# Kernel optimization log

Measured on AMD Instinct MI355X. Metric: run time of the kernel, lower is better.

The kernel has to match this reference:

```python
import jax, jax.numpy as jnp
import numpy as np

B, T, D = 2, 2048, 2048
H, DH = 32, 64
GN_EPS = DH * 1e-5  # GroupNorm eps = head_dim * norm_eps


def _lora(x, A, Bm, bias, act):
    h = x @ A.T
    if act == 'tanh':
        h = jnp.tanh(h)
    elif act == 'sigmoid':
        h = jax.nn.sigmoid(h)
    y = h @ Bm.T
    if bias is not None:
        y = y + bias
    return y


def setup_inputs() -> dict:
    key = jax.random.key(0)
    ks = jax.random.split(key, 24)
    def nrm(i, shape, s):
        return jax.random.normal(ks[i], shape, jnp.float32) * s
    return {
        'hidden_states': nrm(0, (B, T, D), 1.0),
        'v_state': nrm(1, (B, T, D), 1.0),
        'x_x': nrm(2, (6, D), 0.3),
        'k_k': 0.85 + nrm(3, (D,), 0.05),
        'k_a': 1.0 + nrm(4, (D,), 0.05),
        'r_k': nrm(5, (H, DH), 0.1),
        'Wr': nrm(6, (D, D), 0.02),
        'Wk': nrm(7, (D, D), 0.02),
        'Wv': nrm(8, (D, D), 0.02),
        'Wo': nrm(9, (D, D), 0.02),
        'wA': nrm(10, (64, D), 0.02), 'wB': nrm(11, (D, 64), 0.02), 'wb': nrm(12, (D,), 0.5),
        'vA': nrm(13, (16, D), 0.02), 'vB': nrm(14, (D, 16), 0.02), 'vb': jnp.zeros((D,), jnp.float32),
        'aA': nrm(15, (64, D), 0.02), 'aB': nrm(16, (D, 64), 0.02), 'ab': jnp.zeros((D,), jnp.float32),
        'gA': nrm(17, (128, D), 0.02), 'gB': nrm(18, (D, 128), 0.02),
        'gn_w': jnp.ones((D,), jnp.float32), 'gn_b': jnp.zeros((D,), jnp.float32),
    }


def reference(hidden_states, v_state, x_x, k_k, k_a, r_k, Wr, Wk, Wv, Wo,
              wA, wB, wb, vA, vB, vb, aA, aB, ab, gA, gB, gn_w, gn_b):
    b, t, d = hidden_states.shape
    # time_shift: shifted[t] = x[t-1], shifted[0] = 0
    shifted = jnp.pad(hidden_states, ((0, 0), (1, 0), (0, 0)))[:, :t]
    delta = shifted - hidden_states
    xm = hidden_states[None] + delta[None] * x_x[:, None, None, :]  # [6,B,T,D]
    xr, xw, xk, xv, xa, xg = xm[0], xm[1], xm[2], xm[3], xm[4], xm[5]

    r = xr @ Wr.T
    w = -jax.nn.softplus(-_lora(xw, wA, wB, wb, 'tanh')) - 0.5  # log decay, < -0.5
    k = xk @ Wk.T
    v = xv @ Wv.T
    # layer_idx != 0: v = lerp(v, v_state, sigmoid(v_lora(xv)))
    v = v + jax.nn.sigmoid(_lora(xv, vA, vB, vb, None)) * (v_state - v)
    a = jax.nn.sigmoid(_lora(xa, aA, aB, ab, None))
    g = _lora(xg, gA, gB, None, 'sigmoid')

    kk = (k * k_k).reshape(b, t, H, DH)
    kk = kk / jnp.maximum(jnp.linalg.norm(kk, axis=-1, keepdims=True), 1e-12)
    k = k * (1.0 + (a - 1.0) * k_a)

    r_h = r.reshape(b, t, H, DH)
    w_h = w.reshape(b, t, H, DH)
    k_h = k.reshape(b, t, H, DH)
    v_h = v.reshape(b, t, H, DH)
    a_h = a.reshape(b, t, H, DH)
    tm = lambda x: jnp.swapaxes(x, 0, 1)  # [B,T,H,DH] -> [T,B,H,DH]

    # RWKV7 DPLR delta rule: S = diag(exp(w)) S; S += b (a^T S) + k v^T; o = r^T S
    def step(S, xs):
        q_t, w_t, k_t, v_t, at, bt = xs  # each [B,H,DH]
        S = S * jnp.exp(w_t)[..., None]
        sa = jnp.einsum('bhk,bhkv->bhv', at, S)
        S = S + bt[..., None] * sa[..., None, :] + k_t[..., None] * v_t[..., None, :]
        return S, jnp.einsum('bhk,bhkv->bhv', q_t, S)

    S0 = jnp.zeros((b, H, DH, DH), hidden_states.dtype)
    _, o = jax.lax.scan(step, S0,
                        (tm(r_h), tm(w_h), tm(k_h), tm(v_h), tm(-kk), tm(kk * a_h)))
    o = jnp.swapaxes(o, 0, 1)  # [B,T,H,DH]

    # GroupNorm over each head's channels
    mu = o.mean(-1, keepdims=True)
    var = jnp.mean((o - mu) ** 2, axis=-1, keepdims=True)
    on = ((o - mu) / jnp.sqrt(var + GN_EPS)).reshape(b, t, d) * gn_w + gn_b

    on = on + ((r_h * k_h * r_k).sum(-1, keepdims=True) * v_h).reshape(b, t, d)
    return (on * g) @ Wo.T
```

## Files before the change

### kernel.cpp

```cpp
#include <hip/hip_runtime.h>
#include <hip/hip_bf16.h>
#include <math.h>


typedef __attribute__((ext_vector_type(8))) unsigned short ushort8;
typedef __attribute__((ext_vector_type(8))) _Float16 f16x8;
typedef __attribute__((ext_vector_type(4))) float f32x4;
typedef __attribute__((ext_vector_type(2))) float f32x2;

__device__ inline unsigned short f2h(float f) {
    _Float16 h = (_Float16)f;
    return __builtin_bit_cast(unsigned short, h);
}
__device__ inline float h2f(unsigned short u) {
    return (float)__builtin_bit_cast(_Float16, u);
}
__device__ inline float sigm(float x) { return 1.f / (1.f + expf(-x)); }

template <int CTRL>
__device__ __forceinline__ float rrot(float x) {
    int xi = __builtin_bit_cast(int, x);
    int yi = __builtin_amdgcn_update_dpp(xi, xi, CTRL, 0xf, 0xf, true);
    return x + __builtin_bit_cast(float, yi);
}
__device__ __forceinline__ float red8(float x)  { return rrot<0x128>(x); }
__device__ __forceinline__ float red16(float x) {
    float b = x;
    asm("" : "+v"(b));
    float a = x;
    asm("v_permlane16_swap_b32 %0, %1" : "+v"(a), "+v"(b));
    return a + b;
}
__device__ __forceinline__ float red32(float x) {
    float b = x;
    asm("" : "+v"(b));
    float a = x;
    asm("v_permlane32_swap_b32 %0, %1" : "+v"(a), "+v"(b));
    return a + b;
}
__device__ __forceinline__ float full64(float x) {
    x = rrot<0x121>(x);
    x = rrot<0x122>(x);
    x = rrot<0x124>(x);
    x = rrot<0x128>(x);
    return red32(red16(x));
}

__device__ __forceinline__ void gld16(void* lds, const void* g)
{
    __builtin_amdgcn_global_load_lds(
        (const __attribute__((address_space(1))) void*)g,
        (__attribute__((address_space(3))) void*)lds, 16, 0, 0);
}
__device__ __forceinline__ void gld4(void* lds, const void* g)
{
    __builtin_amdgcn_global_load_lds(
        (const __attribute__((address_space(1))) void*)g,
        (__attribute__((address_space(3))) void*)lds, 4, 0, 0);
}

__global__ void mixcvt_h(const float* __restrict__ in, const float* __restrict__ xxr,
                         unsigned short* __restrict__ o16, int T, int D, int total8, int domix)
{
    int i = blockIdx.x * 256 + threadIdx.x;
    if (i >= total8) return;
    const size_t e = (size_t)i * 8;
    float a[8];
    *(float4*)&a[0] = *(const float4*)(in + e);
    *(float4*)&a[4] = *(const float4*)(in + e + 4);
    if (domix) {
        const int m = (int)(e / D);
        const int d = (int)(e % D);
        const int t = m % T;
        float p[8] = {0.f,0.f,0.f,0.f,0.f,0.f,0.f,0.f};
        if (t > 0) {
            *(float4*)&p[0] = *(const float4*)(in + e - D);
            *(float4*)&p[4] = *(const float4*)(in + e - D + 4);
        }
        float xv[8];
        *(float4*)&xv[0] = *(const float4*)(xxr + d);
        *(float4*)&xv[4] = *(const float4*)(xxr + d + 4);
        #pragma unroll
        for (int j = 0; j < 8; ++j) a[j] += (p[j] - a[j]) * xv[j];
    }
    ushort8 o;
    #pragma unroll
    for (int j = 0; j < 8; ++j) o[j] = f2h(a[j]);
    *(ushort8*)(o16 + e) = o;
}

__global__ void mixcvt2_h(const float* __restrict__ in,
                          const float* __restrict__ xx0, const float* __restrict__ xx1,
                          unsigned short* __restrict__ o0, unsigned short* __restrict__ o1,
                          int T, int D, int total8)
{
    int i = blockIdx.x * 256 + threadIdx.x;
    if (i >= total8) return;
    const size_t e = (size_t)i * 8;
    float a[8];
    *(float4*)&a[0] = *(const float4*)(in + e);
    *(float4*)&a[4] = *(const float4*)(in + e + 4);
    const int m = (int)(e / D);
    const int d = (int)(e % D);
    const int t = m % T;
    float p[8] = {0.f,0.f,0.f,0.f,0.f,0.f,0.f,0.f};
    if (t > 0) {
        *(float4*)&p[0] = *(const float4*)(in + e - D);
        *(float4*)&p[4] = *(const float4*)(in + e - D + 4);
    }
    float x0[8], x1[8];
    *(float4*)&x0[0] = *(const float4*)(xx0 + d);
    *(float4*)&x0[4] = *(const float4*)(xx0 + d + 4);
    *(float4*)&x1[0] = *(const float4*)(xx1 + d);
    *(float4*)&x1[4] = *(const float4*)(xx1 + d + 4);
    ushort8 r0, r1;
    #pragma unroll
    for (int j = 0; j < 8; ++j) {
        r0[j] = f2h(a[j] + (p[j] - a[j]) * x0[j]);
        r1[j] = f2h(a[j] + (p[j] - a[j]) * x1[j]);
    }
    *(ushort8*)(o0 + e) = r0;
    *(ushort8*)(o1 + e) = r1;
}

__global__ void wsplit_h(const float* __restrict__ in,
                         unsigned short* __restrict__ hi, unsigned short* __restrict__ lo,
                         int total8)
{
    int i = blockIdx.x * 256 + threadIdx.x;
    if (i >= total8) return;
    const size_t e = (size_t)i * 8;
    float a[8];
    *(float4*)&a[0] = *(const float4*)(in + e);
    *(float4*)&a[4] = *(const float4*)(in + e + 4);
    ushort8 h8, l8;
    #pragma unroll
    for (int j = 0; j < 8; ++j) {
        const unsigned short h = f2h(a[j]);
        h8[j] = h;
        l8[j] = f2h(a[j] - h2f(h));
    }
    *(ushort8*)(hi + e) = h8;
    *(ushort8*)(lo + e) = l8;
}

__global__ void wcvt_h(const float* __restrict__ in,
                       unsigned short* __restrict__ hi, int total8)
{
    int i = blockIdx.x * 256 + threadIdx.x;
    if (i >= total8) return;
    const size_t e = (size_t)i * 8;
    float a[8];
    *(float4*)&a[0] = *(const float4*)(in + e);
    *(float4*)&a[4] = *(const float4*)(in + e + 4);
    ushort8 h8;
    #pragma unroll
    for (int j = 0; j < 8; ++j) h8[j] = f2h(a[j]);
    *(ushort8*)(hi + e) = h8;
}

#define GBM 128
#define GBN 128

template <int TERMS>
__global__ __launch_bounds__(256) void gemm_h2(
    const unsigned short* __restrict__ Ag,
    const unsigned short* __restrict__ Bhg, const unsigned short* __restrict__ Blg,
    float* __restrict__ C, int M, int N, int K, int mode,
    const float* __restrict__ yv, const float* __restrict__ bias,
    const float* __restrict__ aux,
    size_t sA, size_t sB, size_t sC)
{
    __shared__ unsigned short As[GBM * 32];
    __shared__ unsigned short Bhs[GBN * 32], Bls[GBN * 32];
    const int z = blockIdx.z;
    Ag  += (size_t)z * sA;
    Bhg += (size_t)z * sB;
    Blg += (size_t)z * sB;
    C   += (size_t)z * sC;
    const int tid = threadIdx.x;
    const int m0 = blockIdx.x * GBM;
    const int n0 = blockIdx.y * GBN;
    const int wave = tid >> 6, lane = tid & 63;
    const int wr = (wave >> 1) * 64, wc = (wave & 1) * 64;
    const int fr = lane & 15, fq = lane >> 4;

    f32x4 acc[4][4];
    #pragma unroll
    for (int i = 0; i < 4; ++i)
        #pragma unroll
        for (int j = 0; j < 4; ++j)
            acc[i][j] = (f32x4){0.f, 0.f, 0.f, 0.f};

    const unsigned short* gsrc;
    unsigned short* lbuf;
    int rofs, nld;
    if (wave == 0)      { gsrc = Ag;  lbuf = As;           rofs = m0;      nld = 4; }
    else if (wave == 1) { gsrc = Ag;  lbuf = As + 64 * 32; rofs = m0 + 64; nld = 4; }
    else if (wave == 2) { gsrc = Bhg; lbuf = Bhs;          rofs = n0;      nld = 8; }
    else                { gsrc = Blg; lbuf = Bls;          rofs = n0;      nld = (TERMS == 2) ? 8 : 0; }
    const unsigned short* gbase = gsrc + (size_t)(rofs + (lane >> 2)) * K + ((lane & 3) << 3);

    for (int k0 = 0; k0 < K; k0 += 32) {
        #pragma unroll
        for (int j = 0; j < 8; ++j)
            if (j < nld)
                gld16(lbuf + j * 16 * 32, gbase + (size_t)(j * 16) * K + k0);
        __syncthreads();

        f16x8 fa[4], fbh[4], fbl[4];
        #pragma unroll
        for (int m = 0; m < 4; ++m)
            fa[m] = *(const f16x8*)&As[(wr + m * 16 + fr) * 32 + fq * 8];
        #pragma unroll
        for (int n = 0; n < 4; ++n) {
            fbh[n] = *(const f16x8*)&Bhs[(wc + n * 16 + fr) * 32 + fq * 8];
            if constexpr (TERMS == 2)
                fbl[n] = *(const f16x8*)&Bls[(wc + n * 16 + fr) * 32 + fq * 8];
        }
        #pragma unroll
        for (int m = 0; m < 4; ++m)
            #pragma unroll
            for (int n = 0; n < 4; ++n) {
                acc[m][n] = __builtin_amdgcn_mfma_f32_16x16x32_f16(fa[m], fbh[n], acc[m][n], 0, 0, 0);
                if constexpr (TERMS == 2)
                    acc[m][n] = __builtin_amdgcn_mfma_f32_16x16x32_f16(fa[m], fbl[n], acc[m][n], 0, 0, 0);
            }
        __syncthreads();
    }

    #pragma unroll
    for (int m = 0; m < 4; ++m) {
        const int row = m0 + wr + m * 16 + fq * 4;
        #pragma unroll
        for (int n = 0; n < 4; ++n) {
            const int col = n0 + wc + n * 16 + fr;
            #pragma unroll
            for (int j = 0; j < 4; ++j) {
                const size_t idx = (size_t)(row + j) * N + col;
                float v = acc[m][n][j];
                if (mode == 2) {
                    const float sg = sigm(yv[idx] + bias[col]);
                    v = v + sg * (aux[idx] - v);
                }
                C[idx] = v;
            }
        }
    }
}

#define BM 64
#define BN 64
#define BK 16
__global__ __launch_bounds__(256) void gemm_f32(
    const float* __restrict__ A, const float* __restrict__ xx,
    const float* __restrict__ W, float* __restrict__ C,
    int M, int N, int K, int T, int mode, const float* __restrict__ bias)
{
    __shared__ float As[BK][BM + 4];
    __shared__ float Bs[BK][BN + 4];
    const int tid = threadIdx.x;
    const int m0 = blockIdx.x * BM;
    const int n0 = blockIdx.y * BN;
    const int lr = tid >> 2;
    const int lk = (tid & 3) << 2;
    const int tx = tid & 15;
    const int ty = tid >> 4;
    const int mrow = m0 + lr;
    const int nrow = n0 + lr;
    float acc[4][4];
    #pragma unroll
    for (int i = 0; i < 4; ++i)
        #pragma unroll
        for (int j = 0; j < 4; ++j) acc[i][j] = 0.f;

    for (int k0 = 0; k0 < K; k0 += BK) {
        const float* ap = A + (size_t)mrow * K + k0 + lk;
        float4 av = *(const float4*)ap;
        if (xx) {
            const int t = mrow % T;
            float4 pv = make_float4(0.f, 0.f, 0.f, 0.f);
            if (t > 0) pv = *(const float4*)(ap - K);
            const float4 xv = *(const float4*)(xx + k0 + lk);
            av.x += (pv.x - av.x) * xv.x;
            av.y += (pv.y - av.y) * xv.y;
            av.z += (pv.z - av.z) * xv.z;
            av.w += (pv.w - av.w) * xv.w;
        }
        float4 bv = make_float4(0.f, 0.f, 0.f, 0.f);
        if (nrow < N) bv = *(const float4*)(W + (size_t)nrow * K + k0 + lk);

        As[lk + 0][lr] = av.x; As[lk + 1][lr] = av.y;
        As[lk + 2][lr] = av.z; As[lk + 3][lr] = av.w;
        Bs[lk + 0][lr] = bv.x; Bs[lk + 1][lr] = bv.y;
        Bs[lk + 2][lr] = bv.z; Bs[lk + 3][lr] = bv.w;
        __syncthreads();

        #pragma unroll
        for (int kk = 0; kk < BK; ++kk) {
            const float4 a4 = *(const float4*)&As[kk][ty << 2];
            const float4 b4 = *(const float4*)&Bs[kk][tx << 2];
            const float a[4] = {a4.x, a4.y, a4.z, a4.w};
            const float b[4] = {b4.x, b4.y, b4.z, b4.w};
            #pragma unroll
            for (int i = 0; i < 4; ++i)
                #pragma unroll
                for (int j = 0; j < 4; ++j)
                    acc[i][j] = fmaf(a[i], b[j], acc[i][j]);
        }
        __syncthreads();
    }
    #pragma unroll
    for (int i = 0; i < 4; ++i) {
        const int m = m0 + (ty << 2) + i;
        #pragma unroll
        for (int j = 0; j < 4; ++j) {
            const int n = n0 + (tx << 2) + j;
            if (n < N) {
                const size_t idx = (size_t)m * N + n;
                float v = acc[i][j];
                if (mode == 1) v = 0.6065306597126334f * sigm(v + bias[n]);
                C[idx] = v;
            }
        }
    }
}

__global__ __launch_bounds__(256) void lora1(
    const float* __restrict__ hid, const float* __restrict__ x_x,
    const float* __restrict__ wA, const float* __restrict__ vA,
    const float* __restrict__ aA, const float* __restrict__ gA,
    float* __restrict__ HW, float* __restrict__ HV,
    float* __restrict__ HA, float* __restrict__ HG,
    int M, int K, int T)
{
    __shared__ float As[BK][BM + 4];
    __shared__ float Bs[BK][BN + 4];
    const int y = blockIdx.y;
    const float* W; const float* xx; float* C; int NL, act, nofs, nvalid;
    if (y == 0)      { W = wA; xx = x_x + 1 * (size_t)K; C = HW; NL = 64;  act = 1; nofs = 0;  nvalid = 64; }
    else if (y == 1) { W = vA; xx = x_x + 3 * (size_t)K; C = HV; NL = 16;  act = 0; nofs = 0;  nvalid = 16; }
    else if (y == 2) { W = aA; xx = x_x + 4 * (size_t)K; C = HA; NL = 64;  act = 0; nofs = 0;  nvalid = 64; }
    else             { W = gA + (size_t)(y - 3) * 64 * K; xx = x_x + 5 * (size_t)K; C = HG; NL = 128; act = 2; nofs = (y - 3) * 64; nvalid = 64; }

    const int tid = threadIdx.x;
    const int m0 = blockIdx.x * BM;
    const int lr = tid >> 2;
    const int lk = (tid & 3) << 2;
    const int tx = tid & 15;
    const int ty = tid >> 4;
    const int mrow = m0 + lr;
    float acc[4][4];
    #pragma unroll
    for (int i = 0; i < 4; ++i)
        #pragma unroll
        for (int j = 0; j < 4; ++j) acc[i][j] = 0.f;

    for (int k0 = 0; k0 < K; k0 += BK) {
        const float* ap = hid + (size_t)mrow * K + k0 + lk;
        float4 av = *(const float4*)ap;
        {
            const int t = mrow % T;
            float4 pv = make_float4(0.f, 0.f, 0.f, 0.f);
            if (t > 0) pv = *(const float4*)(ap - K);
            const float4 xv = *(const float4*)(xx + k0 + lk);
            av.x += (pv.x - av.x) * xv.x;
            av.y += (pv.y - av.y) * xv.y;
            av.z += (pv.z - av.z) * xv.z;
            av.w += (pv.w - av.w) * xv.w;
        }
        float4 bv = make_float4(0.f, 0.f, 0.f, 0.f);
        if (lr < nvalid) bv = *(const float4*)(W + (size_t)lr * K + k0 + lk);

        As[lk + 0][lr] = av.x; As[lk + 1][lr] = av.y;
        As[lk + 2][lr] = av.z; As[lk + 3][lr] = av.w;
        Bs[lk + 0][lr] = bv.x; Bs[lk + 1][lr] = bv.y;
        Bs[lk + 2][lr] = bv.z; Bs[lk + 3][lr] = bv.w;
        __syncthreads();

        #pragma unroll
        for (int kk = 0; kk < BK; ++kk) {
            const float4 a4 = *(const float4*)&As[kk][ty << 2];
            const float4 b4 = *(const float4*)&Bs[kk][tx << 2];
            const float a[4] = {a4.x, a4.y, a4.z, a4.w};
            const float b[4] = {b4.x, b4.y, b4.z, b4.w};
            #pragma unroll
            for (int i = 0; i < 4; ++i)
                #pragma unroll
                for (int j = 0; j < 4; ++j)
                    acc[i][j] = fmaf(a[i], b[j], acc[i][j]);
        }
        __syncthreads();
    }
    #pragma unroll
    for (int i = 0; i < 4; ++i) {
        const int m = m0 + (ty << 2) + i;
        #pragma unroll
        for (int j = 0; j < 4; ++j) {
            const int n = (tx << 2) + j;
            if (n < nvalid) {
                float v = acc[i][j];
                if (act == 1) v = tanhf(v);
                else if (act == 2) v = sigm(v);
                C[(size_t)m * NL + nofs + n] = v;
            }
        }
    }
}

__global__ __launch_bounds__(256) void ka_epi(
    float* __restrict__ Kf, float* __restrict__ A_BV, float* __restrict__ KKo,
    const float* __restrict__ k_k, const float* __restrict__ k_a,
    const float* __restrict__ ab, int total, int H)
{
    int wid = (blockIdx.x << 2) | (threadIdx.x >> 6);
    if (wid >= total) return;
    const int l = threadIdx.x & 63;
    const int h = wid % H;
    const int ch = h * 64 + l;
    const size_t base = (size_t)wid * 64;
    float k0 = Kf[base + l];
    float a = sigm(A_BV[base + l] + ab[ch]);
    float kkr = k0 * k_k[ch];
    float ss = full64(kkr * kkr);
    float inv = 1.f / fmaxf(sqrtf(ss), 1e-12f);
    float kkn = kkr * inv;
    KKo[base + l] = kkn;
    A_BV[base + l] = kkn * a;
    Kf[base + l] = k0 * fmaf(a - 1.f, k_a[ch], 1.f);
}

#define SCH 16
__global__ __launch_bounds__(64) void rwkv_scan(
    const float* __restrict__ EW, const float* __restrict__ R,
    const float* __restrict__ Kf, const float* __restrict__ Vf,
    const float* __restrict__ KK, const float* __restrict__ BV,
    float* __restrict__ O, int T, int H)
{
    __shared__ float lds[2][5 * SCH * 64 + SCH * 8];

    const int blk = blockIdx.x;
    const int bh = blk & 63;
    const int slab = blk >> 6;
    const int b = bh >> 5, h = bh & 31;
    const int l = threadIdx.x;
    const int vc = l & 7;
    const int g  = l >> 3;
    const int kb = g << 3;
    const int vb0 = slab << 3;
    const size_t step = (size_t)H * 64;
    const size_t base0 = ((size_t)b * T * H + h) * 64;

    auto stage = [&](int c, int buf) {
        float* L = &lds[buf][0];
        const size_t t0 = (size_t)c * SCH;
        const float* gs[5] = {EW, R, Kf, KK, BV};
        #pragma unroll
// ... 47 lines not shown
                const f32x2 qlo = __builtin_shufflevector(pp.q[j], pp.q[j], 0, 1);
                const f32x2 qhi = __builtin_shufflevector(pp.q[j], pp.q[j], 2, 3);
                s2[2*j]   *= elo;
                s2[2*j+1] *= ehi;
                sa0 += qlo * s2[2*j];
                sa1 += qhi * s2[2*j+1];
            }
            const f32x2 sas = sa0 + sa1;
            float p = -(sas.x + sas.y);
            p = red32(red16(red8(p)));
            const f32x2 p2 = (f32x2){p, p};
            const f32x2 v2 = (f32x2){pp.vv, pp.vv};
            f32x2 o0 = (f32x2){0.f, 0.f}, o1 = (f32x2){0.f, 0.f};
            #pragma unroll
            for (int j = 0; j < 2; ++j) {
                const f32x2 klo = __builtin_shufflevector(pp.k[j], pp.k[j], 0, 1);
                const f32x2 khi = __builtin_shufflevector(pp.k[j], pp.k[j], 2, 3);
                const f32x2 blo = __builtin_shufflevector(pp.bb[j], pp.bb[j], 0, 1);
                const f32x2 bhi = __builtin_shufflevector(pp.bb[j], pp.bb[j], 2, 3);
                const f32x2 rlo = __builtin_shufflevector(pp.r[j], pp.r[j], 0, 1);
                const f32x2 rhi = __builtin_shufflevector(pp.r[j], pp.r[j], 2, 3);
                s2[2*j]   = blo * p2 + (klo * v2 + s2[2*j]);
                s2[2*j+1] = bhi * p2 + (khi * v2 + s2[2*j+1]);
                o0 += rlo * s2[2*j];
                o1 += rhi * s2[2*j+1];
            }
            const f32x2 os = o0 + o1;
            float oo = os.x + os.y;
            oo = red32(red16(red8(oo)));
            if (g == 0)
                O[base0 + (size_t)(c * SCH + tt) * step + vb0 + vc] = oo;
        };

        PRE(PA, 0);
        PRE(PB, 1);
        #pragma unroll
        for (int tt = 0; tt < SCH - 2; tt += 2) {
            COMP(PA, tt);     PRE(PA, tt + 2);
            COMP(PB, tt + 1); PRE(PB, tt + 3);
        }
        COMP(PA, SCH - 2);
        COMP(PB, SCH - 1);

        asm volatile("s_waitcnt vmcnt(0)" ::: "memory");
        __builtin_amdgcn_sched_barrier(0);
    }
}

__global__ __launch_bounds__(256) void gn_bonus(
    const float* __restrict__ O, const float* __restrict__ R,
    const float* __restrict__ Kf, const float* __restrict__ Vf,
    const float* __restrict__ G, const float* __restrict__ r_k,
    const float* __restrict__ gn_w, const float* __restrict__ gn_b,
    float* __restrict__ ON, int total, int H, float eps)
{
    int wid = (blockIdx.x << 2) | (threadIdx.x >> 6);
    if (wid >= total) return;
    const int l = threadIdx.x & 63;
    const int h = wid % H;
    const int ch = h * 64 + l;
    const size_t base = (size_t)wid * 64;

    const float o = O[base + l];
    const float mu = full64(o) * (1.f / 64.f);
    const float d = o - mu;
    const float ss = full64(d * d);
    const float inv = 1.f / sqrtf(ss * (1.f / 64.f) + eps);
    float on = d * inv * gn_w[ch] + gn_b[ch];

    const float r = R[base + l], k = Kf[base + l], vv = Vf[base + l];
    const float p = full64(r * k * r_k[ch]);
    on = fmaf(p, vv, on);
    ON[base + l] = on * G[base + l];
}

extern "C" void kernel_launch(void* const* d_in, const int* in_sizes, int n_in,
                              void* d_out, int out_size, void* d_ws, size_t ws_size,
                              hipStream_t stream)
{
    const int B = 2, T = 2048, D = 2048, H = 32;
    const int M = B * T;

    const float* hid = (const float*)d_in[0];
    const float* vst = (const float*)d_in[1];
    const float* x_x = (const float*)d_in[2];
    const float* k_k = (const float*)d_in[3];
    const float* k_a = (const float*)d_in[4];
    const float* r_k = (const float*)d_in[5];
    const float* Wr  = (const float*)d_in[6];
    const float* Wk  = (const float*)d_in[7];
    const float* Wv  = (const float*)d_in[8];
    const float* Wo  = (const float*)d_in[9];
    const float* wA  = (const float*)d_in[10];
    const float* wB  = (const float*)d_in[11];
    const float* wb  = (const float*)d_in[12];
    const float* vA  = (const float*)d_in[13];
    const float* vB  = (const float*)d_in[14];
    const float* vb  = (const float*)d_in[15];
    const float* aA  = (const float*)d_in[16];
    const float* aB  = (const float*)d_in[17];
    const float* ab  = (const float*)d_in[18];
    const float* gA  = (const float*)d_in[19];
    const float* gB  = (const float*)d_in[20];
    const float* gnw = (const float*)d_in[21];
    const float* gnb = (const float*)d_in[22];
    float* out = (float*)d_out;

    const size_t NE = (size_t)M * D;
    const size_t DD = (size_t)D * D;
    const size_t need = (6 * NE + (size_t)M * 272) * sizeof(float);
    if (ws_size < need) return;

    float* R_  = (float*)d_ws;
    float* EW  = R_  + NE;
    float* Kf  = EW  + NE;
    float* Vf  = Kf  + NE;
    float* KK  = Vf  + NE;
    float* ABV = KK  + NE;
    float* HW  = ABV + NE;
    float* HV  = HW + (size_t)M * 64;
    float* HA  = HV + (size_t)M * 16;
    float* HG  = HA + (size_t)M * 64;

    dim3 blk(256);
    const int nMix = (int)(NE / 8);
    const int nW   = (int)(DD / 8);
    const float* nf = nullptr;

    hipLaunchKernelGGL(lora1, dim3(M / BM, 5), blk, 0, stream,
                       hid, x_x, wA, vA, aA, gA, HW, HV, HA, HG, M, D, T);

    hipLaunchKernelGGL(gemm_f32, dim3(M / BM, D / BN), blk, 0, stream, HV, nf, vB, ABV, M, D, 16, T, 0, nf);

    unsigned short* X2  = (unsigned short*)EW;
    unsigned short* W2  = (unsigned short*)KK;
    hipLaunchKernelGGL(mixcvt2_h, dim3(nMix / 256), blk, 0, stream,
                       hid, x_x + 0 * (size_t)D, x_x + 2 * (size_t)D, X2, X2 + NE, T, D, nMix);
    hipLaunchKernelGGL(wcvt_h, dim3(nW / 256), blk, 0, stream, Wr, W2, nW);
    hipLaunchKernelGGL(wcvt_h, dim3(nW / 256), blk, 0, stream, Wk, W2 + DD, nW);
    hipLaunchKernelGGL((gemm_h2<1>), dim3(M / GBM, D / GBN, 2), blk, 0, stream,
                       X2, W2, W2, R_, M, D, D, 0, nf, nf, nf,
                       NE, DD, 2 * NE);

    hipLaunchKernelGGL(mixcvt_h, dim3(nMix / 256), blk, 0, stream, hid, x_x + 3 * (size_t)D, X2, T, D, nMix, 1);
    hipLaunchKernelGGL(wcvt_h, dim3(nW / 256), blk, 0, stream, Wv, W2, nW);
    hipLaunchKernelGGL((gemm_h2<1>), dim3(M / GBM, D / GBN, 1), blk, 0, stream,
                       X2, W2, W2, Vf, M, D, D, 2, ABV, vb, vst, 0, 0, 0);

    hipLaunchKernelGGL(gemm_f32, dim3(M / BM, D / BN), blk, 0, stream, HW, nf, wB, EW,  M, D, 64, T, 1, wb);
    hipLaunchKernelGGL(gemm_f32, dim3(M / BM, D / BN), blk, 0, stream, HA, nf, aB, ABV, M, D, 64, T, 0, nf);

    const int totalW = M * H;
    hipLaunchKernelGGL(ka_epi, dim3(totalW / 4), blk, 0, stream, Kf, ABV, KK, k_k, k_a, ab, totalW, H);

    hipLaunchKernelGGL(rwkv_scan, dim3(B * H * 8), dim3(64), 0, stream, EW, R_, Kf, Vf, KK, ABV, out, T, H);

    unsigned short* HG16 = (unsigned short*)ABV;
    unsigned short* gbHi = HG16 + (size_t)M * 128;
    unsigned short* gbLo = gbHi + (size_t)D * 128;
    float* G_ = KK;
    hipLaunchKernelGGL(mixcvt_h, dim3((M * 128 / 8) / 256), blk, 0, stream, HG, nf, HG16, T, D, M * 128 / 8, 0);
    hipLaunchKernelGGL(wsplit_h, dim3((D * 128 / 8) / 256), blk, 0, stream, gB, gbHi, gbLo, D * 128 / 8);
    hipLaunchKernelGGL((gemm_h2<2>), dim3(M / GBM, D / GBN, 1), blk, 0, stream,
                       HG16, gbHi, gbLo, G_, M, D, 128, 0, nf, nf, nf, 0, 0, 0);
    hipLaunchKernelGGL(gn_bonus, dim3(totalW / 4), blk, 0, stream, out, R_, Kf, Vf, G_, r_k, gnw, gnb, EW, totalW, H, 64.f * 1e-5f);

    unsigned short* ON16 = (unsigned short*)KK;
    unsigned short* WoHi = (unsigned short*)ABV;
    unsigned short* WoLo = WoHi + DD;
    hipLaunchKernelGGL(mixcvt_h, dim3(nMix / 256), blk, 0, stream, EW, nf, ON16, T, D, nMix, 0);
    hipLaunchKernelGGL(wsplit_h, dim3(nW / 256), blk, 0, stream, Wo, WoHi, WoLo, nW);
    hipLaunchKernelGGL((gemm_h2<2>), dim3(M / GBM, D / GBN, 1), blk, 0, stream,
                       ON16, WoHi, WoLo, out, M, D, D, 0, nf, nf, nf, 0, 0, 0);
}
```

Measured before the change: 1.005 ms.

## Fuse fp16 conversions into producer epilogues and batch small kernels

The gate-LoRA hidden state is now written as fp16 straight from lora1, and gn_bonus writes its output as fp16. This removes two separate mixcvt conversion passes and the fp32 round trip through memory that each one needed. The two weight conversions for Wr/Wk are merged into one launch, and the w/a LoRA second-stage GEMMs run in one launch using a z-grid. Buffer aliasing is reshuffled so ON16 lives in EW and HG16 sits in the small workspace region.

```diff
diff --git a/kernel.cpp b/kernel.cpp
--- a/kernel.cpp
+++ b/kernel.cpp
@@ -144,11 +144,14 @@
     *(ushort8*)(lo + e) = l8;
 }
 
-__global__ void wcvt_h(const float* __restrict__ in,
-                       unsigned short* __restrict__ hi, int total8)
+__global__ void wcvt2_h(const float* __restrict__ in0, const float* __restrict__ in1,
+                        unsigned short* __restrict__ hi0, unsigned short* __restrict__ hi1,
+                        int total8)
 {
     int i = blockIdx.x * 256 + threadIdx.x;
     if (i >= total8) return;
+    const float* in = (blockIdx.y == 0) ? in0 : in1;
+    unsigned short* hi = (blockIdx.y == 0) ? hi0 : hi1;
     const size_t e = (size_t)i * 8;
     float a[8];
     *(float4*)&a[0] = *(const float4*)(in + e);
@@ -326,22 +329,89 @@
     }
 }
 
+__global__ __launch_bounds__(256) void lora2_pair(
+    const float* __restrict__ HW, const float* __restrict__ wBw, const float* __restrict__ wb,
+    const float* __restrict__ HA, const float* __restrict__ aBw,
+    float* __restrict__ EW, float* __restrict__ YA,
+    int M, int N, int K)
+{
+    __shared__ float As[BK][BM + 4];
+    __shared__ float Bs[BK][BN + 4];
+    const int z = blockIdx.z;
+    const float* A = (z == 0) ? HW : HA;
+    const float* W = (z == 0) ? wBw : aBw;
+    float* C = (z == 0) ? EW : YA;
+    const int tid = threadIdx.x;
+    const int m0 = blockIdx.x * BM;
+    const int n0 = blockIdx.y * BN;
+    const int lr = tid >> 2;
+    const int lk = (tid & 3) << 2;
+    const int tx = tid & 15;
+    const int ty = tid >> 4;
+    const int mrow = m0 + lr;
+    const int nrow = n0 + lr;
+    float acc[4][4];
+    #pragma unroll
+    for (int i = 0; i < 4; ++i)
+        #pragma unroll
+        for (int j = 0; j < 4; ++j) acc[i][j] = 0.f;
+
+    for (int k0 = 0; k0 < K; k0 += BK) {
+        const float* ap = A + (size_t)mrow * K + k0 + lk;
+        const float4 av = *(const float4*)ap;
+        float4 bv = make_float4(0.f, 0.f, 0.f, 0.f);
+        if (nrow < N) bv = *(const float4*)(W + (size_t)nrow * K + k0 + lk);
+
+        As[lk + 0][lr] = av.x; As[lk + 1][lr] = av.y;
+        As[lk + 2][lr] = av.z; As[lk + 3][lr] = av.w;
+        Bs[lk + 0][lr] = bv.x; Bs[lk + 1][lr] = bv.y;
+        Bs[lk + 2][lr] = bv.z; Bs[lk + 3][lr] = bv.w;
+        __syncthreads();
+
+        #pragma unroll
+        for (int kk = 0; kk < BK; ++kk) {
+            const float4 a4 = *(const float4*)&As[kk][ty << 2];
+            const float4 b4 = *(const float4*)&Bs[kk][tx << 2];
+            const float a[4] = {a4.x, a4.y, a4.z, a4.w};
+            const float b[4] = {b4.x, b4.y, b4.z, b4.w};
+            #pragma unroll
+            for (int i = 0; i < 4; ++i)
+                #pragma unroll
+                for (int j = 0; j < 4; ++j)
+                    acc[i][j] = fmaf(a[i], b[j], acc[i][j]);
+        }
+        __syncthreads();
+    }
+    #pragma unroll
+    for (int i = 0; i < 4; ++i) {
+        const int m = m0 + (ty << 2) + i;
+        #pragma unroll
+        for (int j = 0; j < 4; ++j) {
+            const int n = n0 + (tx << 2) + j;
+            const size_t idx = (size_t)m * N + n;
+            float v = acc[i][j];
+            if (z == 0) v = 0.6065306597126334f * sigm(v + wb[n]);
+            C[idx] = v;
+        }
+    }
+}
+
 __global__ __launch_bounds__(256) void lora1(
     const float* __restrict__ hid, const float* __restrict__ x_x,
     const float* __restrict__ wA, const float* __restrict__ vA,
     const float* __restrict__ aA, const float* __restrict__ gA,
     float* __restrict__ HW, float* __restrict__ HV,
-    float* __restrict__ HA, float* __restrict__ HG,
+    float* __restrict__ HA, unsigned short* __restrict__ HG16,
     int M, int K, int T)
 {
     __shared__ float As[BK][BM + 4];
     __shared__ float Bs[BK][BN + 4];
     const int y = blockIdx.y;
-    const float* W; const float* xx; float* C; int NL, act, nofs, nvalid;
-    if (y == 0)      { W = wA; xx = x_x + 1 * (size_t)K; C = HW; NL = 64;  act = 1; nofs = 0;  nvalid = 64; }
-    else if (y == 1) { W = vA; xx = x_x + 3 * (size_t)K; C = HV; NL = 16;  act = 0; nofs = 0;  nvalid = 16; }
-    else if (y == 2) { W = aA; xx = x_x + 4 * (size_t)K; C = HA; NL = 64;  act = 0; nofs = 0;  nvalid = 64; }
-    else             { W = gA + (size_t)(y - 3) * 64 * K; xx = x_x + 5 * (size_t)K; C = HG; NL = 128; act = 2; nofs = (y - 3) * 64; nvalid = 64; }
+    const float* W; const float* xx; int act, nofs, nvalid;
+    if (y == 0)      { W = wA; xx = x_x + 1 * (size_t)K; act = 1; nofs = 0;  nvalid = 64; }
+    else if (y == 1) { W = vA; xx = x_x + 3 * (size_t)K; act = 0; nofs = 0;  nvalid = 16; }
+    else if (y == 2) { W = aA; xx = x_x + 4 * (size_t)K; act = 0; nofs = 0;  nvalid = 64; }
+    else             { W = gA + (size_t)(y - 3) * 64 * K; xx = x_x + 5 * (size_t)K; act = 2; nofs = (y - 3) * 64; nvalid = 64; }
 
     const int tid = threadIdx.x;
     const int m0 = blockIdx.x * BM;
@@ -400,9 +470,10 @@
             const int n = (tx << 2) + j;
             if (n < nvalid) {
                 float v = acc[i][j];
-                if (act == 1) v = tanhf(v);
-                else if (act == 2) v = sigm(v);
-                C[(size_t)m * NL + nofs + n] = v;
+                if (act == 1) { HW[(size_t)m * 64 + n] = tanhf(v); }
+                else if (act == 2) { HG16[(size_t)m * 128 + nofs + n] = f2h(sigm(v)); }
+                else if (y == 1) { HV[(size_t)m * 16 + n] = v; }
+                else { HA[(size_t)m * 64 + n] = v; }
             }
         }
     }
@@ -556,7 +627,7 @@
     const float* __restrict__ Kf, const float* __restrict__ Vf,
     const float* __restrict__ G, const float* __restrict__ r_k,
     const float* __restrict__ gn_w, const float* __restrict__ gn_b,
-    float* __restrict__ ON, int total, int H, float eps)
+    unsigned short* __restrict__ ON16, int total, int H, float eps)
 {
     int wid = (blockIdx.x << 2) | (threadIdx.x >> 6);
     if (wid >= total) return;
@@ -575,7 +646,7 @@
     const float r = R[base + l], k = Kf[base + l], vv = Vf[base + l];
     const float p = full64(r * k * r_k[ch]);
     on = fmaf(p, vv, on);
-    ON[base + l] = on * G[base + l];
+    ON16[base + l] = f2h(on * G[base + l]);
 }
 
 extern "C" void kernel_launch(void* const* d_in, const int* in_sizes, int n_in,
@@ -624,7 +695,7 @@
     float* HW  = ABV + NE;
     float* HV  = HW + (size_t)M * 64;
     float* HA  = HV + (size_t)M * 16;
-    float* HG  = HA + (size_t)M * 64;
+    unsigned short* HG16 = (unsigned short*)(HA + (size_t)M * 64);
 
     dim3 blk(256);
     const int nMix = (int)(NE / 8);
@@ -632,7 +703,7 @@
     const float* nf = nullptr;
 
     hipLaunchKernelGGL(lora1, dim3(M / BM, 5), blk, 0, stream,
-                       hid, x_x, wA, vA, aA, gA, HW, HV, HA, HG, M, D, T);
+                       hid, x_x, wA, vA, aA, gA, HW, HV, HA, HG16, M, D, T);
 
     hipLaunchKernelGGL(gemm_f32, dim3(M / BM, D / BN), blk, 0, stream, HV, nf, vB, ABV, M, D, 16, T, 0, nf);
 
@@ -640,39 +711,36 @@
     unsigned short* W2  = (unsigned short*)KK;
     hipLaunchKernelGGL(mixcvt2_h, dim3(nMix / 256), blk, 0, stream,
                        hid, x_x + 0 * (size_t)D, x_x + 2 * (size_t)D, X2, X2 + NE, T, D, nMix);
-    hipLaunchKernelGGL(wcvt_h, dim3(nW / 256), blk, 0, stream, Wr, W2, nW);
-    hipLaunchKernelGGL(wcvt_h, dim3(nW / 256), blk, 0, stream, Wk, W2 + DD, nW);
+    hipLaunchKernelGGL(wcvt2_h, dim3(nW / 256, 2), blk, 0, stream, Wr, Wk, W2, W2 + DD, nW);
     hipLaunchKernelGGL((gemm_h2<1>), dim3(M / GBM, D / GBN, 2), blk, 0, stream,
                        X2, W2, W2, R_, M, D, D, 0, nf, nf, nf,
                        NE, DD, 2 * NE);
 
     hipLaunchKernelGGL(mixcvt_h, dim3(nMix / 256), blk, 0, stream, hid, x_x + 3 * (size_t)D, X2, T, D, nMix, 1);
-    hipLaunchKernelGGL(wcvt_h, dim3(nW / 256), blk, 0, stream, Wv, W2, nW);
+    hipLaunchKernelGGL(wcvt2_h, dim3(nW / 256, 1), blk, 0, stream, Wv, Wv, W2, W2, nW);
     hipLaunchKernelGGL((gemm_h2<1>), dim3(M / GBM, D / GBN, 1), blk, 0, stream,
                        X2, W2, W2, Vf, M, D, D, 2, ABV, vb, vst, 0, 0, 0);
 
-    hipLaunchKernelGGL(gemm_f32, dim3(M / BM, D / BN), blk, 0, stream, HW, nf, wB, EW,  M, D, 64, T, 1, wb);
-    hipLaunchKernelGGL(gemm_f32, dim3(M / BM, D / BN), blk, 0, stream, HA, nf, aB, ABV, M, D, 64, T, 0, nf);
+    hipLaunchKernelGGL(lora2_pair, dim3(M / BM, D / BN, 2), blk, 0, stream,
+                       HW, wB, wb, HA, aB, EW, ABV, M, D, 64);
 
     const int totalW = M * H;
     hipLaunchKernelGGL(ka_epi, dim3(totalW / 4), blk, 0, stream, Kf, ABV, KK, k_k, k_a, ab, totalW, H);
 
     hipLaunchKernelGGL(rwkv_scan, dim3(B * H * 8), dim3(64), 0, stream, EW, R_, Kf, Vf, KK, ABV, out, T, H);
 
-    unsigned short* HG16 = (unsigned short*)ABV;
-    unsigned short* gbHi = HG16 + (size_t)M * 128;
+    unsigned short* gbHi = (unsigned short*)ABV;
     unsigned short* gbLo = gbHi + (size_t)D * 128;
     float* G_ = KK;
-    hipLaunchKernelGGL(mixcvt_h, dim3((M * 128 / 8) / 256), blk, 0, stream, HG, nf, HG16, T, D, M * 128 / 8, 0);
     hipLaunchKernelGGL(wsplit_h, dim3((D * 128 / 8) / 256), blk, 0, stream, gB, gbHi, gbLo, D * 128 / 8);
     hipLaunchKernelGGL((gemm_h2<2>), dim3(M / GBM, D / GBN, 1), blk, 0, stream,
                        HG16, gbHi, gbLo, G_, M, D, 128, 0, nf, nf, nf, 0, 0, 0);
-    hipLaunchKernelGGL(gn_bonus, dim3(totalW / 4), blk, 0, stream, out, R_, Kf, Vf, G_, r_k, gnw, gnb, EW, totalW, H, 64.f * 1e-5f);
-
-    unsigned short* ON16 = (unsigned short*)KK;
+
+    unsigned short* ON16 = (unsigned short*)EW;
+    hipLaunchKernelGGL(gn_bonus, dim3(totalW / 4), blk, 0, stream, out, R_, Kf, Vf, G_, r_k, gnw, gnb, ON16, totalW, H, 64.f * 1e-5f);
+
     unsigned short* WoHi = (unsigned short*)ABV;
     unsigned short* WoLo = WoHi + DD;
-    hipLaunchKernelGGL(mixcvt_h, dim3(nMix / 256), blk, 0, stream, EW, nf, ON16, T, D, nMix, 0);
     hipLaunchKernelGGL(wsplit_h, dim3(nW / 256), blk, 0, stream, Wo, WoHi, WoLo, nW);
     hipLaunchKernelGGL((gemm_h2<2>), dim3(M / GBM, D / GBN, 1), blk, 0, stream,
                        ON16, WoHi, WoLo, out, M, D, D, 0, nf, nf, nf, 0, 0, 0);
```

Measured after the change: 984.3 us. -2.1%, faster.

## Move LoRA down-projections and B-projections to fp16 MFMA, fuse mixes and conversions

Applied to the files above, without the earlier changes.

Replaces the fp32 FMA LoRA-A kernel with an MFMA fp16 GEMM over pre-mixed fp16 inputs, with weights zero-padded to 128 rows. The w and a LoRA-B projections now run as one batched fp16 MFMA GEMM, with the decay activation fused into the epilogue. Four token-mix outputs are produced by one kernel, the Wr/Wk conversions are merged, and gn_bonus writes fp16 directly so a separate conversion pass is dropped. The aim is to cut slow scalar-FP32 GEMM time and launch count, at the cost of fp16 rounding in the LoRA paths and a heavily reshuffled workspace aliasing scheme.

```diff
diff --git a/kernel.cpp b/kernel.cpp
--- a/kernel.cpp
+++ b/kernel.cpp
@@ -57,36 +57,6 @@
     __builtin_amdgcn_global_load_lds(
         (const __attribute__((address_space(1))) void*)g,
         (__attribute__((address_space(3))) void*)lds, 4, 0, 0);
-}
-
-__global__ void mixcvt_h(const float* __restrict__ in, const float* __restrict__ xxr,
-                         unsigned short* __restrict__ o16, int T, int D, int total8, int domix)
-{
-    int i = blockIdx.x * 256 + threadIdx.x;
-    if (i >= total8) return;
-    const size_t e = (size_t)i * 8;
-    float a[8];
-    *(float4*)&a[0] = *(const float4*)(in + e);
-    *(float4*)&a[4] = *(const float4*)(in + e + 4);
-    if (domix) {
-        const int m = (int)(e / D);
-        const int d = (int)(e % D);
-        const int t = m % T;
-        float p[8] = {0.f,0.f,0.f,0.f,0.f,0.f,0.f,0.f};
-        if (t > 0) {
-            *(float4*)&p[0] = *(const float4*)(in + e - D);
-            *(float4*)&p[4] = *(const float4*)(in + e - D + 4);
-        }
-        float xv[8];
-        *(float4*)&xv[0] = *(const float4*)(xxr + d);
-        *(float4*)&xv[4] = *(const float4*)(xxr + d + 4);
-        #pragma unroll
-        for (int j = 0; j < 8; ++j) a[j] += (p[j] - a[j]) * xv[j];
-    }
-    ushort8 o;
-    #pragma unroll
-    for (int j = 0; j < 8; ++j) o[j] = f2h(a[j]);
-    *(ushort8*)(o16 + e) = o;
 }
 
 __global__ void mixcvt2_h(const float* __restrict__ in,
@@ -123,6 +93,44 @@
     *(ushort8*)(o1 + e) = r1;
 }
 
+__global__ void mixcvt4_h(const float* __restrict__ in, const float* __restrict__ x_x,
+                          unsigned short* __restrict__ ow, unsigned short* __restrict__ oa,
+                          unsigned short* __restrict__ og, unsigned short* __restrict__ ov,
+                          int T, int D, int total8)
+{
+    int i = blockIdx.x * 256 + threadIdx.x;
+    if (i >= total8) return;
+    const size_t e = (size_t)i * 8;
+    float a[8];
+    *(float4*)&a[0] = *(const float4*)(in + e);
+    *(float4*)&a[4] = *(const float4*)(in + e + 4);
+    const int m = (int)(e / D);
+    const int d = (int)(e % D);
+    const int t = m % T;
+    float p[8] = {0.f,0.f,0.f,0.f,0.f,0.f,0.f,0.f};
+    if (t > 0) {
+        *(float4*)&p[0] = *(const float4*)(in + e - D);
+        *(float4*)&p[4] = *(const float4*)(in + e - D + 4);
+    }
+    const float* xxw = x_x + 1 * (size_t)D + d;
+    const float* xxa = x_x + 4 * (size_t)D + d;
+    const float* xxg = x_x + 5 * (size_t)D + d;
+    const float* xxv = x_x + 3 * (size_t)D + d;
+    ushort8 rw, ra, rg, rv;
+    #pragma unroll
+    for (int j = 0; j < 8; ++j) {
+        const float dl = p[j] - a[j];
+        rw[j] = f2h(a[j] + dl * xxw[j]);
+        ra[j] = f2h(a[j] + dl * xxa[j]);
+        rg[j] = f2h(a[j] + dl * xxg[j]);
+        rv[j] = f2h(a[j] + dl * xxv[j]);
+    }
+    *(ushort8*)(ow + e) = rw;
+    *(ushort8*)(oa + e) = ra;
+    *(ushort8*)(og + e) = rg;
+    *(ushort8*)(ov + e) = rv;
+}
+
 __global__ void wsplit_h(const float* __restrict__ in,
                          unsigned short* __restrict__ hi, unsigned short* __restrict__ lo,
                          int total8)
@@ -144,11 +152,14 @@
     *(ushort8*)(lo + e) = l8;
 }
 
-__global__ void wcvt_h(const float* __restrict__ in,
-                       unsigned short* __restrict__ hi, int total8)
+__global__ void wcvt2_h(const float* __restrict__ in0, const float* __restrict__ in1,
+                        unsigned short* __restrict__ hi0, unsigned short* __restrict__ hi1,
+                        int total8)
 {
     int i = blockIdx.x * 256 + threadIdx.x;
     if (i >= total8) return;
+    const float* in = (blockIdx.y == 0) ? in0 : in1;
+    unsigned short* hi = (blockIdx.y == 0) ? hi0 : hi1;
     const size_t e = (size_t)i * 8;
     float a[8];
     *(float4*)&a[0] = *(const float4*)(in + e);
@@ -157,6 +168,31 @@
     #pragma unroll
     for (int j = 0; j < 8; ++j) h8[j] = f2h(a[j]);
     *(ushort8*)(hi + e) = h8;
+}
+
+__global__ void wcvt_lora(const float* __restrict__ wA, const float* __restrict__ vA,
+                          const float* __restrict__ aA, const float* __restrict__ gA,
+                          unsigned short* __restrict__ WL, int K)
+{
+    const int z = blockIdx.y;
+    int i = blockIdx.x * 256 + threadIdx.x;
+    const size_t e = (size_t)i * 8;
+    const int row = (int)(e / K);
+    const int col = (int)(e % K);
+    const int nv = (z == 0) ? 64 : (z == 1) ? 16 : (z == 2) ? 64 : 128;
+    const float* src = (z == 0) ? wA : (z == 1) ? vA : (z == 2) ? aA : gA;
+    ushort8 h8;
+    if (row < nv) {
+        float a[8];
+        *(float4*)&a[0] = *(const float4*)(src + (size_t)row * K + col);
+        *(float4*)&a[4] = *(const float4*)(src + (size_t)row * K + col + 4);
+        #pragma unroll
+        for (int j = 0; j < 8; ++j) h8[j] = f2h(a[j]);
+    } else {
+        #pragma unroll
+        for (int j = 0; j < 8; ++j) h8[j] = 0;
+    }
+    *(ushort8*)(WL + (size_t)z * 128 * K + e) = h8;
 }
 
 #define GBM 128
@@ -242,8 +278,86 @@
                 if (mode == 2) {
                     const float sg = sigm(yv[idx] + bias[col]);
                     v = v + sg * (aux[idx] - v);
+                } else if (mode == 3 && z == 0) {
+                    v = 0.6065306597126334f * sigm(v + bias[col]);
                 }
                 C[idx] = v;
+            }
+        }
+    }
+}
+
+__global__ __launch_bounds__(256) void lora1_h(
+    const unsigned short* __restrict__ Xbase,
+    const unsigned short* __restrict__ WL,
+    unsigned short* __restrict__ HW16, float* __restrict__ HV,
+    unsigned short* __restrict__ HA16, unsigned short* __restrict__ HG16,
+    int M, int K, size_t NE)
+{
+    __shared__ unsigned short As[GBM * 32];
+    __shared__ unsigned short Bhs[GBN * 32];
+    const int z = blockIdx.z;
+    const size_t zofs = (z == 0) ? 0 : (z == 1) ? 3 * NE : (z == 2) ? NE : 2 * NE;
+    const unsigned short* Ag = Xbase + zofs;
+    const unsigned short* Bg = WL + (size_t)z * 128 * K;
+    const int tid = threadIdx.x;
+    const int m0 = blockIdx.x * GBM;
+    const int wave = tid >> 6, lane = tid & 63;
+    const int wr = (wave >> 1) * 64, wc = (wave & 1) * 64;
+    const int fr = lane & 15, fq = lane >> 4;
+
+    f32x4 acc[4][4];
+    #pragma unroll
+    for (int i = 0; i < 4; ++i)
+        #pragma unroll
+        for (int j = 0; j < 4; ++j)
+            acc[i][j] = (f32x4){0.f, 0.f, 0.f, 0.f};
+
+    const unsigned short* gsrc;
+    unsigned short* lbuf;
+    int rofs, nld;
+    if (wave == 0)      { gsrc = Ag; lbuf = As;           rofs = m0;      nld = 4; }
+    else if (wave == 1) { gsrc = Ag; lbuf = As + 64 * 32; rofs = m0 + 64; nld = 4; }
+    else if (wave == 2) { gsrc = Bg; lbuf = Bhs;          rofs = 0;       nld = 8; }
+    else                { gsrc = Bg; lbuf = Bhs;          rofs = 0;       nld = 0; }
+    const unsigned short* gbase = gsrc + (size_t)(rofs + (lane >> 2)) * K + ((lane & 3) << 3);
+
+    for (int k0 = 0; k0 < K; k0 += 32) {
+        #pragma unroll
+        for (int j = 0; j < 8; ++j)
+            if (j < nld)
+                gld16(lbuf + j * 16 * 32, gbase + (size_t)(j * 16) * K + k0);
+        __syncthreads();
+
+        f16x8 fa[4], fb[4];
+        #pragma unroll
+        for (int m = 0; m < 4; ++m)
+            fa[m] = *(const f16x8*)&As[(wr + m * 16 + fr) * 32 + fq * 8];
+        #pragma unroll
+        for (int n = 0; n < 4; ++n)
+            fb[n] = *(const f16x8*)&Bhs[(wc + n * 16 + fr) * 32 + fq * 8];
+        #pragma unroll
+        for (int m = 0; m < 4; ++m)
+            #pragma unroll
+            for (int n = 0; n < 4; ++n)
+                acc[m][n] = __builtin_amdgcn_mfma_f32_16x16x32_f16(fa[m], fb[n], acc[m][n], 0, 0, 0);
+        __syncthreads();
+    }
+
+    #pragma unroll
+    for (int m = 0; m < 4; ++m) {
+        const int row = m0 + wr + m * 16 + fq * 4;
+        #pragma unroll
+        for (int n = 0; n < 4; ++n) {
+            const int col = wc + n * 16 + fr;
+            #pragma unroll
+            for (int j = 0; j < 4; ++j) {
+                const float v = acc[m][n][j];
+                const int r = row + j;
+                if (z == 0)      { if (col < 64) HW16[(size_t)r * 64 + col] = f2h(tanhf(v)); }
+                else if (z == 1) { if (col < 16) HV[(size_t)r * 16 + col] = v; }
+                else if (z == 2) { if (col < 64) HA16[(size_t)r * 64 + col] = f2h(v); }
+                else             { HG16[(size_t)r * 128 + col] = f2h(sigm(v)); }
             }
         }
     }
@@ -321,88 +435,6 @@
                 float v = acc[i][j];
                 if (mode == 1) v = 0.6065306597126334f * sigm(v + bias[n]);
                 C[idx] = v;
-            }
-        }
-    }
-}
-
-__global__ __launch_bounds__(256) void lora1(
-    const float* __restrict__ hid, const float* __restrict__ x_x,
-    const float* __restrict__ wA, const float* __restrict__ vA,
-    const float* __restrict__ aA, const float* __restrict__ gA,
-    float* __restrict__ HW, float* __restrict__ HV,
-    float* __restrict__ HA, float* __restrict__ HG,
-    int M, int K, int T)
-{
-    __shared__ float As[BK][BM + 4];
-    __shared__ float Bs[BK][BN + 4];
-    const int y = blockIdx.y;
-    const float* W; const float* xx; float* C; int NL, act, nofs, nvalid;
-    if (y == 0)      { W = wA; xx = x_x + 1 * (size_t)K; C = HW; NL = 64;  act = 1; nofs = 0;  nvalid = 64; }
-    else if (y == 1) { W = vA; xx = x_x + 3 * (size_t)K; C = HV; NL = 16;  act = 0; nofs = 0;  nvalid = 16; }
-    else if (y == 2) { W = aA; xx = x_x + 4 * (size_t)K; C = HA; NL = 64;  act = 0; nofs = 0;  nvalid = 64; }
-    else             { W = gA + (size_t)(y - 3) * 64 * K; xx = x_x + 5 * (size_t)K; C = HG; NL = 128; act = 2; nofs = (y - 3) * 64; nvalid = 64; }
-
-    const int tid = threadIdx.x;
-    const int m0 = blockIdx.x * BM;
-    const int lr = tid >> 2;
-    const int lk = (tid & 3) << 2;
-    const int tx = tid & 15;
-    const int ty = tid >> 4;
-    const int mrow = m0 + lr;
-    float acc[4][4];
-    #pragma unroll
-    for (int i = 0; i < 4; ++i)
-        #pragma unroll
-        for (int j = 0; j < 4; ++j) acc[i][j] = 0.f;
-
-    for (int k0 = 0; k0 < K; k0 += BK) {
-        const float* ap = hid + (size_t)mrow * K + k0 + lk;
-        float4 av = *(const float4*)ap;
-        {
-            const int t = mrow % T;
-            float4 pv = make_float4(0.f, 0.f, 0.f, 0.f);
-            if (t > 0) pv = *(const float4*)(ap - K);
-            const float4 xv = *(const float4*)(xx + k0 + lk);
-            av.x += (pv.x - av.x) * xv.x;
-            av.y += (pv.y - av.y) * xv.y;
-            av.z += (pv.z - av.z) * xv.z;
-            av.w += (pv.w - av.w) * xv.w;
-        }
-        float4 bv = make_float4(0.f, 0.f, 0.f, 0.f);
-        if (lr < nvalid) bv = *(const float4*)(W + (size_t)lr * K + k0 + lk);
-
-        As[lk + 0][lr] = av.x; As[lk + 1][lr] = av.y;
-        As[lk + 2][lr] = av.z; As[lk + 3][lr] = av.w;
-        Bs[lk + 0][lr] = bv.x; Bs[lk + 1][lr] = bv.y;
-        Bs[lk + 2][lr] = bv.z; Bs[lk + 3][lr] = bv.w;
-        __syncthreads();
-
-        #pragma unroll
-        for (int kk = 0; kk < BK; ++kk) {
-            const float4 a4 = *(const float4*)&As[kk][ty << 2];
-            const float4 b4 = *(const float4*)&Bs[kk][tx << 2];
-            const float a[4] = {a4.x, a4.y, a4.z, a4.w};
-            const float b[4] = {b4.x, b4.y, b4.z, b4.w};
-            #pragma unroll
-            for (int i = 0; i < 4; ++i)
-                #pragma unroll
-                for (int j = 0; j < 4; ++j)
-                    acc[i][j] = fmaf(a[i], b[j], acc[i][j]);
-        }
-        __syncthreads();
-    }
-    #pragma unroll
-    for (int i = 0; i < 4; ++i) {
-        const int m = m0 + (ty << 2) + i;
-        #pragma unroll
-        for (int j = 0; j < 4; ++j) {
-            const int n = (tx << 2) + j;
-            if (n < nvalid) {
-                float v = acc[i][j];
-                if (act == 1) v = tanhf(v);
-                else if (act == 2) v = sigm(v);
-                C[(size_t)m * NL + nofs + n] = v;
             }
         }
     }
@@ -556,7 +588,7 @@
     const float* __restrict__ Kf, const float* __restrict__ Vf,
     const float* __restrict__ G, const float* __restrict__ r_k,
     const float* __restrict__ gn_w, const float* __restrict__ gn_b,
-    float* __restrict__ ON, int total, int H, float eps)
+    unsigned short* __restrict__ ON16, int total, int H, float eps)
 {
     int wid = (blockIdx.x << 2) | (threadIdx.x >> 6);
     if (wid >= total) return;
@@ -575,7 +607,7 @@
     const float r = R[base + l], k = Kf[base + l], vv = Vf[base + l];
     const float p = full64(r * k * r_k[ch]);
     on = fmaf(p, vv, on);
-    ON[base + l] = on * G[base + l];
+    ON16[base + l] = f2h(on * G[base + l]);
 }
 
 extern "C" void kernel_launch(void* const* d_in, const int* in_sizes, int n_in,
@@ -615,64 +647,73 @@
     const size_t need = (6 * NE + (size_t)M * 272) * sizeof(float);
     if (ws_size < need) return;
 
-    float* R_  = (float*)d_ws;
-    float* EW  = R_  + NE;
-    float* Kf  = EW  + NE;
-    float* Vf  = Kf  + NE;
-    float* KK  = Vf  + NE;
-    float* ABV = KK  + NE;
-    float* HW  = ABV + NE;
-    float* HV  = HW + (size_t)M * 64;
-    float* HA  = HV + (size_t)M * 16;
-    float* HG  = HA + (size_t)M * 64;
+    float* W0 = (float*)d_ws;
+    float* W1 = W0 + NE;
+    float* W2 = W1 + NE;
+    float* W3 = W2 + NE;
+    float* W4 = W3 + NE;
+    float* W5 = W4 + NE;
+    float* SMALL = W5 + NE;
+    unsigned short* HW16 = (unsigned short*)SMALL;
+    unsigned short* HA16 = HW16 + (size_t)M * 64;
+    unsigned short* HG16 = HA16 + (size_t)M * 64;
+    float* HV = (float*)(HG16 + (size_t)M * 128);
 
     dim3 blk(256);
     const int nMix = (int)(NE / 8);
     const int nW   = (int)(DD / 8);
     const float* nf = nullptr;
 
-    hipLaunchKernelGGL(lora1, dim3(M / BM, 5), blk, 0, stream,
-                       hid, x_x, wA, vA, aA, gA, HW, HV, HA, HG, M, D, T);
-
-    hipLaunchKernelGGL(gemm_f32, dim3(M / BM, D / BN), blk, 0, stream, HV, nf, vB, ABV, M, D, 16, T, 0, nf);
-
-    unsigned short* X2  = (unsigned short*)EW;
-    unsigned short* W2  = (unsigned short*)KK;
+    unsigned short* X2   = (unsigned short*)W1;
+    unsigned short* X4   = (unsigned short*)W4;
+    unsigned short* WRK  = (unsigned short*)W3;
+    unsigned short* WL   = (unsigned short*)W0;
+
     hipLaunchKernelGGL(mixcvt2_h, dim3(nMix / 256), blk, 0, stream,
                        hid, x_x + 0 * (size_t)D, x_x + 2 * (size_t)D, X2, X2 + NE, T, D, nMix);
-    hipLaunchKernelGGL(wcvt_h, dim3(nW / 256), blk, 0, stream, Wr, W2, nW);
-    hipLaunchKernelGGL(wcvt_h, dim3(nW / 256), blk, 0, stream, Wk, W2 + DD, nW);
+    hipLaunchKernelGGL(mixcvt4_h, dim3(nMix / 256), blk, 0, stream,
+                       hid, x_x, X4, X4 + NE, X4 + 2 * NE, X4 + 3 * NE, T, D, nMix);
+
+    hipLaunchKernelGGL(wcvt2_h, dim3(nW / 256, 2), blk, 0, stream, Wr, Wk, WRK, WRK + DD, nW);
+    hipLaunchKernelGGL(wcvt_lora, dim3(128, 4), blk, 0, stream, wA, vA, aA, gA, WL, D);
+
+    hipLaunchKernelGGL(lora1_h, dim3(M / GBM, 1, 4), blk, 0, stream,
+                       X4, WL, HW16, HV, HA16, HG16, M, D, NE);
+
     hipLaunchKernelGGL((gemm_h2<1>), dim3(M / GBM, D / GBN, 2), blk, 0, stream,
-                       X2, W2, W2, R_, M, D, D, 0, nf, nf, nf,
+                       X2, WRK, WRK, W0, M, D, D, 0, nf, nf, nf,
                        NE, DD, 2 * NE);
 
-    hipLaunchKernelGGL(mixcvt_h, dim3(nMix / 256), blk, 0, stream, hid, x_x + 3 * (size_t)D, X2, T, D, nMix, 1);
-    hipLaunchKernelGGL(wcvt_h, dim3(nW / 256), blk, 0, stream, Wv, W2, nW);
+    hipLaunchKernelGGL(gemm_f32, dim3(M / BM, D / BN), blk, 0, stream, HV, nf, vB, W1, M, D, 16, T, 0, nf);
+
+    unsigned short* WvH = (unsigned short*)W4;
+    hipLaunchKernelGGL(wcvt2_h, dim3(nW / 256, 1), blk, 0, stream, Wv, Wv, WvH, WvH, nW);
     hipLaunchKernelGGL((gemm_h2<1>), dim3(M / GBM, D / GBN, 1), blk, 0, stream,
-                       X2, W2, W2, Vf, M, D, D, 2, ABV, vb, vst, 0, 0, 0);
-
-    hipLaunchKernelGGL(gemm_f32, dim3(M / BM, D / BN), blk, 0, stream, HW, nf, wB, EW,  M, D, 64, T, 1, wb);
-    hipLaunchKernelGGL(gemm_f32, dim3(M / BM, D / BN), blk, 0, stream, HA, nf, aB, ABV, M, D, 64, T, 0, nf);
+                       X4 + 3 * NE, WvH, WvH, W3, M, D, D, 2, W1, vb, vst, 0, 0, 0);
+
+    unsigned short* wB16 = (unsigned short*)W4;
+    unsigned short* aB16 = wB16 + (size_t)D * 64;
+    hipLaunchKernelGGL(wcvt2_h, dim3((int)(D * 64 / 8 / 256), 2), blk, 0, stream, wB, aB, wB16, aB16, (int)(D * 64 / 8));
+    hipLaunchKernelGGL((gemm_h2<1>), dim3(M / GBM, D / GBN, 2), blk, 0, stream,
+                       HW16, wB16, wB16, W1, M, D, 64, 3, nf, wb, nf,
+                       (size_t)M * 64, (size_t)D * 64, 4 * NE);
 
     const int totalW = M * H;
-    hipLaunchKernelGGL(ka_epi, dim3(totalW / 4), blk, 0, stream, Kf, ABV, KK, k_k, k_a, ab, totalW, H);
-
-    hipLaunchKernelGGL(rwkv_scan, dim3(B * H * 8), dim3(64), 0, stream, EW, R_, Kf, Vf, KK, ABV, out, T, H);
-
-    unsigned short* HG16 = (unsigned short*)ABV;
-    unsigned short* gbHi = HG16 + (size_t)M * 128;
+    hipLaunchKernelGGL(ka_epi, dim3(totalW / 4), blk, 0, stream, W2, W5, W4, k_k, k_a, ab, totalW, H);
+
+    hipLaunchKernelGGL(rwkv_scan, dim3(B * H * 8), dim3(64), 0, stream, W1, W0, W2, W3, W4, W5, out, T, H);
+
+    unsigned short* gbHi = (unsigned short*)W5;
     unsigned short* gbLo = gbHi + (size_t)D * 128;
-    float* G_ = KK;
-    hipLaunchKernelGGL(mixcvt_h, dim3((M * 128 / 8) / 256), blk, 0, stream, HG, nf, HG16, T, D, M * 128 / 8, 0);
-    hipLaunchKernelGGL(wsplit_h, dim3((D * 128 / 8) / 256), blk, 0, stream, gB, gbHi, gbLo, D * 128 / 8);
+    hipLaunchKernelGGL(wsplit_h, dim3((int)(D * 128 / 8 / 256)), blk, 0, stream, gB, gbHi, gbLo, (int)(D * 128 / 8));
     hipLaunchKernelGGL((gemm_h2<2>), dim3(M / GBM, D / GBN, 1), blk, 0, stream,
-                       HG16, gbHi, gbLo, G_, M, D, 128, 0, nf, nf, nf, 0, 0, 0);
-    hipLaunchKernelGGL(gn_bonus, dim3(totalW / 4), blk, 0, stream, out, R_, Kf, Vf, G_, r_k, gnw, gnb, EW, totalW, H, 64.f * 1e-5f);
-
-    unsigned short* ON16 = (unsigned short*)KK;
-    unsigned short* WoHi = (unsigned short*)ABV;
+                       HG16, gbHi, gbLo, W4, M, D, 128, 0, nf, nf, nf, 0, 0, 0);
+
+    unsigned short* ON16 = (unsigned short*)W1;
+    hipLaunchKernelGGL(gn_bonus, dim3(totalW / 4), blk, 0, stream, out, W0, W2, W3, W4, r_k, gnw, gnb, ON16, totalW, H, 64.f * 1e-5f);
+
+    unsigned short* WoHi = (unsigned short*)W3;
     unsigned short* WoLo = WoHi + DD;
-    hipLaunchKernelGGL(mixcvt_h, dim3(nMix / 256), blk, 0, stream, EW, nf, ON16, T, D, nMix, 0);
     hipLaunchKernelGGL(wsplit_h, dim3(nW / 256), blk, 0, stream, Wo, WoHi, WoLo, nW);
     hipLaunchKernelGGL((gemm_h2<2>), dim3(M / GBM, D / GBN, 1), blk, 0, stream,
                        ON16, WoHi, WoLo, out, M, D, D, 0, nf, nf, nf, 0, 0, 0);
```

New measurement: 918.3 us. -8.6%, faster.
